# Performance work log

Measured on AMD Instinct MI355X. Metric: run time of the kernel, lower is better.

The kernel has to match this reference:

```python
import jax, jax.numpy as jnp
import numpy as np

N_TREE = 200
DEPTH = 3
N_LEAF = 2 ** (DEPTH + 1) - 1      # 15 internal decision nodes
N_LEAVES = N_LEAF + 1              # 16 leaves
N_NODE = 64
BATCH = 2048
D_FEAT = 512
LR = 0.01


def _leaf_paths(depth):
    """For each of the 2^(depth+1) leaves, the internal-node index and the
    left/right bit at every level (matches the tf.gather index construction:
    bit==0 -> take p, bit==1 -> take 1-p; children of node n are 2n+1, 2n+2)."""
    L = 2 ** (depth + 1)
    nodes = np.zeros((L, depth + 1), np.int32)
    bits = np.zeros((L, depth + 1), np.int32)
    for l in range(L):
        node = 0
        for d in range(depth + 1):
            bit = (l >> (depth - d)) & 1
            nodes[l, d] = node
            bits[l, d] = bit
            node = 2 * node + 1 + bit
    return nodes, bits

_NODES, _BITS = _leaf_paths(DEPTH)


def setup_inputs() -> dict:
    key = jax.random.key(0)
    ks = jax.random.split(key, 9)
    u = lambda k, s: jax.random.uniform(k, s, jnp.float32, -0.05, 0.05)  # keras 'uniform' init
    return {
        "x": jax.random.normal(ks[0], (BATCH, D_FEAT), jnp.float32),
        "y_true": jax.random.normal(ks[1], (BATCH, 1), jnp.float32),
        "w_t": u(ks[2], (N_TREE, D_FEAT, N_NODE)),
        "b_t": u(ks[3], (N_TREE, N_NODE)),
        "w_d": u(ks[4], (N_TREE, N_NODE, N_LEAF)),
        "b_d": u(ks[5], (N_TREE, N_LEAF)),
        "w_l": u(ks[6], (N_TREE, N_LEAVES)),
        "b_l": u(ks[7], (N_TREE,)),
        "f_0": jnp.full((1,), 0.5, jnp.float32),
    }


def reference(x, y_true, w_t, b_t, w_d, b_d, w_l, b_l, f_0):
    B = x.shape[0]
    # Batched per-tree small MLP (the 200-iteration Python loop in the original).
    # Dropout is identity at inference.
    h = jax.nn.relu(jnp.einsum('bd,tdn->tbn', x, w_t) + b_t[:, None, :])        # [T,B,N_NODE]
    p = jax.nn.sigmoid(jnp.einsum('tbn,tnl->tbl', h, w_d) + b_d[:, None, :])    # [T,B,15]
    # Soft binary-tree routing: mu[t,b,leaf] = prod over path of p or (1-p).
    # This reproduces the tiled-index tf.gather construction exactly.
    pn = p[..., _NODES]                                                         # [T,B,16,DEPTH+1]
    q = jnp.where(_BITS == 1, 1.0 - pn, pn)
    mu = jnp.prod(q, axis=-1)                                                   # [T,B,16]
    # Per-tree leaf score with tanh.
    f = jnp.tanh(jnp.einsum('tbl,tl->tb', mu, w_l) + b_l[:, None])              # [T,B]
    # Sequential boosting accumulation: predict_k = f_0 + lr * sum_{i<k} f_i.
    cum = f_0 + LR * jnp.cumsum(f.T, axis=1)                                    # [B,T]
    py_x = jnp.concatenate([jnp.broadcast_to(f_0[None, :], (B, 1)), cum], axis=1)  # [B,T+1]
    return py_x
```

## Files before the change

### kernel.cpp

```cpp
#include <hip/hip_runtime.h>

#define T_TREES 200
#define BATCH   2048
#define D_FEAT  512
#define N_NODE  64
#define LR      0.01f

typedef __attribute__((__ext_vector_type__(8)))  __bf16 bf16x8;
typedef __attribute__((__ext_vector_type__(16))) float  f32x16;

__device__ __forceinline__ unsigned short f32_to_bf16(float f) {
    unsigned u = __float_as_uint(f);
    u += 0x7FFFu + ((u >> 16) & 1u);
    return (unsigned short)(u >> 16);
}

__device__ __forceinline__ void gload_lds16(const void* g, void* l) {
    __builtin_amdgcn_global_load_lds(
        (__attribute__((address_space(1))) void*)(void*)g,
        (__attribute__((address_space(3))) void*)l,
        16, 0, 0);
}

__global__ __launch_bounds__(256) void prep_all(
    const float* __restrict__ x, const float* __restrict__ w_t,
    const float* __restrict__ w_d,
    unsigned short* __restrict__ x_p, unsigned short* __restrict__ w_p,
    unsigned short* __restrict__ w_dt) {
    __shared__ float tile[64 * 65];
    int b = blockIdx.x;
    if (b < 256) {
        int mb = b >> 3, slab = b & 7;
        const float* src = x + (mb * 64) * D_FEAT + slab * 64;
        #pragma unroll
        for (int p = 0; p < 16; ++p) {
            int idx = p * 256 + threadIdx.x;
            int r = idx >> 6, c = idx & 63;
            tile[r * 65 + c] = src[r * D_FEAT + c];
        }
        __syncthreads();
        int mt = mb >> 1, mq = mb & 1;
        unsigned short* dst = x_p + mt * 65536 + slab * 8192 + mq * 512;
        #pragma unroll
        for (int p = 0; p < 2; ++p) {
            int sid = p * 256 + threadIdx.x;
            int kgl = sid >> 6;
            int r   = sid & 63;
            const float* sr = &tile[r * 65 + kgl * 8];
            bf16x8 o;
            #pragma unroll
            for (int j = 0; j < 8; ++j) o[j] = (__bf16)sr[j];
            *(bf16x8*)(dst + kgl * 1024 + r * 8) = o;
        }
    } else if (b < 1856) {
        int bb = b - 256;
        int t = bb >> 3, slab = bb & 7;
        const float* src = w_t + t * (D_FEAT * N_NODE) + slab * 64 * N_NODE;
        #pragma unroll
        for (int p = 0; p < 16; ++p) {
            int idx = p * 256 + threadIdx.x;
            int d = idx >> 6, n = idx & 63;
            tile[d * 65 + n] = src[d * N_NODE + n];
        }
        __syncthreads();
        unsigned short* dst = w_p + (t >> 1) * 65536 + slab * 8192 + (t & 1) * 512;
        #pragma unroll
        for (int p = 0; p < 2; ++p) {
            int sid = p * 256 + threadIdx.x;
            int kgl = sid >> 6;
            int n   = sid & 63;
            bf16x8 o;
            #pragma unroll
            for (int j = 0; j < 8; ++j) o[j] = (__bf16)tile[(kgl * 8 + j) * 65 + n];
            *(bf16x8*)(dst + kgl * 1024 + n * 8) = o;
        }
    } else {
        int i = (b - 1856) * 256 + threadIdx.x;
        int n = i & 63;
        int l = (i >> 6) & 31;
        int t = i >> 11;
        float v = (l < 15) ? w_d[(t * 64 + n) * 15 + l] : 0.f;
        w_dt[i] = f32_to_bf16(v);
    }
}

__global__ __launch_bounds__(256, 4) void gbdt_main(
    const unsigned short* __restrict__ x_p,
    const unsigned short* __restrict__ w_p,
    const unsigned short* __restrict__ w_dt,
    const float* __restrict__ b_t,
    const float* __restrict__ b_d,
    const float* __restrict__ w_l,
    const float* __restrict__ b_l,
    float* __restrict__ f_ws)
{
    __shared__ alignas(16) char smem[34816];
    unsigned short* Hs = (unsigned short*)smem;
    __bf16*         Hb = (__bf16*)smem;
    float*          Pf = (float*)smem;

    const int tid    = threadIdx.x;
    const int lane   = tid & 63;
    const int w      = tid >> 6;
    const int lane31 = lane & 31;
    const int kh     = lane >> 5;
    const int wm     = w >> 1;
    const int wn     = w & 1;

    const int xcd  = blockIdx.x & 7;
    const int slot = blockIdx.x >> 3;
    const int mt   = slot & 15;
    const int pj   = slot >> 4;
    const int pair = xcd * 13 + pj;
    if (pair >= 100) return;
    const int t0 = pair * 2;
    const int m0 = mt * 128;

    const unsigned short* pA = x_p + mt * 65536 + kh * 1024 + (wm * 64 + lane31) * 8;
    const char* gb = (const char*)(w_p + pair * 65536) + tid * 16;

    const int boff = kh * 2048 + (wn * 64 + lane31) * 16;

    f32x16 acc[2][2];
    #pragma unroll
    for (int mb = 0; mb < 2; ++mb)
        #pragma unroll
        for (int nb = 0; nb < 2; ++nb)
            acc[mb][nb] = (f32x16)(0.f);

#define LOAD_A(cn, areg) do {                                      \
        _Pragma("unroll")                                          \
        for (int s2 = 0; s2 < 2; ++s2)                             \
            _Pragma("unroll")                                      \
            for (int mb = 0; mb < 2; ++mb)                         \
                (areg)[s2 * 2 + mb] =                              \
                    *(const bf16x8*)(pA + (cn) * 4096 + s2 * 2048 + mb * 256); \
    } while (0)

#define STAGE_B(cn, base) do {                                            \
        gload_lds16(gb + (cn) * 8192,        (base) + tid * 16);          \
        gload_lds16(gb + (cn) * 8192 + 4096, (base) + tid * 16 + 4096);   \
    } while (0)

    bf16x8 aC[4], aN[4];
    LOAD_A(0, aC);
    STAGE_B(0, smem);
    STAGE_B(1, smem + 8192);

    char* rd  = smem;
    char* rd1 = smem + 8192;
    char* st2 = smem + 16384;

    #pragma unroll
    for (int c = 0; c < 16; ++c) {
        if (c < 15) asm volatile("s_waitcnt vmcnt(2)" ::: "memory");
        else        asm volatile("s_waitcnt vmcnt(0)" ::: "memory");
        __builtin_amdgcn_s_barrier();
        if (c < 15) LOAD_A(c + 1, aN);
        if (c < 14) STAGE_B(c + 2, st2);
        __builtin_amdgcn_s_setprio(1);
        #pragma unroll
        for (int s2 = 0; s2 < 2; ++s2) {
            bf16x8 bv0 = *(const bf16x8*)(rd + boff + s2 * 4096);
            bf16x8 bv1 = *(const bf16x8*)(rd + boff + s2 * 4096 + 512);
            acc[0][0] = __builtin_amdgcn_mfma_f32_32x32x16_bf16(aC[s2 * 2 + 0], bv0, acc[0][0], 0, 0, 0);
            acc[0][1] = __builtin_amdgcn_mfma_f32_32x32x16_bf16(aC[s2 * 2 + 0], bv1, acc[0][1], 0, 0, 0);
            acc[1][0] = __builtin_amdgcn_mfma_f32_32x32x16_bf16(aC[s2 * 2 + 1], bv0, acc[1][0], 0, 0, 0);
            acc[1][1] = __builtin_amdgcn_mfma_f32_32x32x16_bf16(aC[s2 * 2 + 1], bv1, acc[1][1], 0, 0, 0);
        }
        __builtin_amdgcn_s_setprio(0);
        char* t = rd; rd = rd1; rd1 = st2; st2 = t;
        #pragma unroll
        for (int i = 0; i < 4; ++i) aC[i] = aN[i];
    }

    __syncthreads();

    #pragma unroll
    for (int nb = 0; nb < 2; ++nb) {
        float btv = b_t[(t0 + wn) * 64 + nb * 32 + lane31];
        #pragma unroll
        for (int mb = 0; mb < 2; ++mb)
            #pragma unroll
            for (int r = 0; r < 16; ++r) {
                int m = wm * 64 + mb * 32 + (r & 3) + 8 * (r >> 2) + 4 * kh;
                float h = fmaxf(acc[mb][nb][r] + btv, 0.f);
                Hb[wn * 8704 + m * 68 + nb * 32 + lane31] = (__bf16)h;
            }
    }
    __syncthreads();

    f32x16 acc2[2] = { (f32x16)(0.f), (f32x16)(0.f) };
    const unsigned short* pW = w_dt + (t0 + wn) * 2048 + lane31 * 64 + kh * 8;
    __builtin_amdgcn_s_setprio(1);
    #pragma unroll
    for (int s = 0; s < 4; ++s) {
        bf16x8 bv = *(const bf16x8*)(pW + s * 16);
        #pragma unroll
        for (int i = 0; i < 2; ++i) {
            const unsigned short* pH =
                Hs + wn * 8704 + (wm * 64 + i * 32 + lane31) * 68 + s * 16 + kh * 8;
            bf16x8 av = *(const bf16x8*)pH;
            acc2[i] = __builtin_amdgcn_mfma_f32_32x32x16_bf16(av, bv, acc2[i], 0, 0, 0);
        }
    }
    __builtin_amdgcn_s_setprio(0);
    __syncthreads();

    if (lane31 < 15) {
        float bdv = b_d[(t0 + wn) * 15 + lane31];
        #pragma unroll
        for (int i = 0; i < 2; ++i)
            #pragma unroll
            for (int r = 0; r < 16; ++r) {
                int m = wm * 64 + i * 32 + (r & 3) + 8 * (r >> 2) + 4 * kh;
                float lg = acc2[i][r] + bdv;
                Pf[(wn * 128 + m) * 17 + lane31] = 1.f / (1.f + __expf(-lg));
            }
    }
    __syncthreads();

    {
        int m = tid & 127;
        int j = tid >> 7;
        int t = t0 + j;
        float pv[15];
        #pragma unroll
        for (int i = 0; i < 15; ++i) pv[i] = Pf[(j * 128 + m) * 17 + i];
        float facc = 0.f;
        #pragma unroll
        for (int leaf = 0; leaf < 16; ++leaf) {
            float mu = 1.f;
            int node = 0;
            #pragma unroll
            for (int d = 0; d < 4; ++d) {
                int bit = (leaf >> (3 - d)) & 1;
                float p = pv[node];
                mu *= bit ? (1.f - p) : p;
                node = 2 * node + 1 + bit;
            }
            facc += mu * w_l[t * 16 + leaf];
        }
        f_ws[(m0 + m) * T_TREES + t] = tanhf(facc + b_l[t]);
    }
#undef STAGE_B
#undef LOAD_A
}

__global__ __launch_bounds__(256) void scan_k(const float* __restrict__ f_ws,
                                              const float* __restrict__ f0p,
                                              float* __restrict__ out) {
    int lane = threadIdx.x & 63, wid = threadIdx.x >> 6;
    int b = blockIdx.x * 4 + wid;
    float f0 = f0p[0];
    float4 v;
    if (lane < 50) v = *(const float4*)(f_ws + b * T_TREES + lane * 4);
    else           v = make_float4(0.f, 0.f, 0.f, 0.f);
    float p0 = v.x;
    float p1 = p0 + v.y;
    float p2 = p1 + v.z;
    float p3 = p2 + v.w;
    float s = p3;
    #pragma unroll
    for (int off = 1; off < 64; off <<= 1) {
        float y = __shfl_up(s, off, 64);
        if (lane >= off) s += y;
    }
    float excl = s - p3;
    if (lane < 50) {
        float* o = out + b * (T_TREES + 1) + 1 + lane * 4;
        o[0] = f0 + LR * (excl + p0);
        o[1] = f0 + LR * (excl + p1);
        o[2] = f0 + LR * (excl + p2);
        o[3] = f0 + LR * (excl + p3);
    }
    if (lane == 0) out[b * (T_TREES + 1)] = f0;
}

extern "C" void kernel_launch(void* const* d_in, const int* in_sizes, int n_in,
                              void* d_out, int out_size, void* d_ws, size_t ws_size,
                              hipStream_t stream) {
    const float* x   = (const float*)d_in[0];
    const float* w_t = (const float*)d_in[2];
    const float* b_t = (const float*)d_in[3];
    const float* w_d = (const float*)d_in[4];
    const float* b_d = (const float*)d_in[5];
    const float* w_l = (const float*)d_in[6];
    const float* b_l = (const float*)d_in[7];
    const float* f_0 = (const float*)d_in[8];
    float* out = (float*)d_out;

    char* ws = (char*)d_ws;
    unsigned short* x_p  = (unsigned short*)(ws);
    unsigned short* w_p  = (unsigned short*)(ws + 2097152);
    unsigned short* w_dt = (unsigned short*)(ws + 15204352);
    float*          f_ws = (float*)(ws + 16023552);

    prep_all<<<3456, 256, 0, stream>>>(x, w_t, w_d, x_p, w_p, w_dt);
    gbdt_main<<<1664, 256, 0, stream>>>(x_p, w_p, w_dt, b_t, b_d, w_l, b_l, f_ws);
    scan_k<<<512, 256, 0, stream>>>(f_ws, f_0, out);
}
```

Measured before the change: 132.0 us.

## Double the batch rows per block to reuse staged tree weights twice

Each block now covers 256 batch rows instead of 128. Every wave holds four M sub-tiles in registers, so each weight tile staged into LDS feeds twice as many MFMAs, and the grid is halved. The epilogue (bias/relu, second matmul, sigmoid, tree routing, tanh) runs in two halves reusing the same LDS buffers, with output rows remapped to match. Launch bounds drop to two blocks per SM to allow the larger accumulator set, which lowers occupancy and adds register pressure.

```diff
diff --git a/kernel.cpp b/kernel.cpp
--- a/kernel.cpp
+++ b/kernel.cpp
@@ -84,7 +84,7 @@
     }
 }
 
-__global__ __launch_bounds__(256, 4) void gbdt_main(
+__global__ __launch_bounds__(256, 2) void gbdt_main(
     const unsigned short* __restrict__ x_p,
     const unsigned short* __restrict__ w_p,
     const unsigned short* __restrict__ w_dt,
@@ -109,21 +109,21 @@
 
     const int xcd  = blockIdx.x & 7;
     const int slot = blockIdx.x >> 3;
-    const int mt   = slot & 15;
-    const int pj   = slot >> 4;
+    const int mt8  = slot & 7;
+    const int pj   = slot >> 3;
     const int pair = xcd * 13 + pj;
     if (pair >= 100) return;
     const int t0 = pair * 2;
-    const int m0 = mt * 128;
-
-    const unsigned short* pA = x_p + mt * 65536 + kh * 1024 + (wm * 64 + lane31) * 8;
+    const int m0 = mt8 * 256;
+
+    const unsigned short* pA = x_p + (2 * mt8 + wm) * 65536 + kh * 1024 + lane31 * 8;
     const char* gb = (const char*)(w_p + pair * 65536) + tid * 16;
 
     const int boff = kh * 2048 + (wn * 64 + lane31) * 16;
 
-    f32x16 acc[2][2];
-    #pragma unroll
-    for (int mb = 0; mb < 2; ++mb)
+    f32x16 acc[4][2];
+    #pragma unroll
+    for (int mb = 0; mb < 4; ++mb)
         #pragma unroll
         for (int nb = 0; nb < 2; ++nb)
             acc[mb][nb] = (f32x16)(0.f);
@@ -132,8 +132,8 @@
         _Pragma("unroll")                                          \
         for (int s2 = 0; s2 < 2; ++s2)                             \
             _Pragma("unroll")                                      \
-            for (int mb = 0; mb < 2; ++mb)                         \
-                (areg)[s2 * 2 + mb] =                              \
+            for (int mb = 0; mb < 4; ++mb)                         \
+                (areg)[s2 * 4 + mb] =                              \
                     *(const bf16x8*)(pA + (cn) * 4096 + s2 * 2048 + mb * 256); \
     } while (0)
 
@@ -142,7 +142,7 @@
         gload_lds16(gb + (cn) * 8192 + 4096, (base) + tid * 16 + 4096);   \
     } while (0)
 
-    bf16x8 aC[4], aN[4];
+    bf16x8 aC[8], aN[8];
     LOAD_A(0, aC);
     STAGE_B(0, smem);
     STAGE_B(1, smem + 8192);
@@ -163,85 +163,97 @@
         for (int s2 = 0; s2 < 2; ++s2) {
             bf16x8 bv0 = *(const bf16x8*)(rd + boff + s2 * 4096);
             bf16x8 bv1 = *(const bf16x8*)(rd + boff + s2 * 4096 + 512);
-            acc[0][0] = __builtin_amdgcn_mfma_f32_32x32x16_bf16(aC[s2 * 2 + 0], bv0, acc[0][0], 0, 0, 0);
-            acc[0][1] = __builtin_amdgcn_mfma_f32_32x32x16_bf16(aC[s2 * 2 + 0], bv1, acc[0][1], 0, 0, 0);
-            acc[1][0] = __builtin_amdgcn_mfma_f32_32x32x16_bf16(aC[s2 * 2 + 1], bv0, acc[1][0], 0, 0, 0);
-            acc[1][1] = __builtin_amdgcn_mfma_f32_32x32x16_bf16(aC[s2 * 2 + 1], bv1, acc[1][1], 0, 0, 0);
+            #pragma unroll
+            for (int mb = 0; mb < 4; ++mb) {
+                acc[mb][0] = __builtin_amdgcn_mfma_f32_32x32x16_bf16(aC[s2 * 4 + mb], bv0, acc[mb][0], 0, 0, 0);
+                acc[mb][1] = __builtin_amdgcn_mfma_f32_32x32x16_bf16(aC[s2 * 4 + mb], bv1, acc[mb][1], 0, 0, 0);
+            }
         }
         __builtin_amdgcn_s_setprio(0);
         char* t = rd; rd = rd1; rd1 = st2; st2 = t;
         #pragma unroll
-        for (int i = 0; i < 4; ++i) aC[i] = aN[i];
+        for (int i = 0; i < 8; ++i) aC[i] = aN[i];
     }
 
     __syncthreads();
 
-    #pragma unroll
-    for (int nb = 0; nb < 2; ++nb) {
-        float btv = b_t[(t0 + wn) * 64 + nb * 32 + lane31];
-        #pragma unroll
-        for (int mb = 0; mb < 2; ++mb)
-            #pragma unroll
-            for (int r = 0; r < 16; ++r) {
-                int m = wm * 64 + mb * 32 + (r & 3) + 8 * (r >> 2) + 4 * kh;
-                float h = fmaxf(acc[mb][nb][r] + btv, 0.f);
-                Hb[wn * 8704 + m * 68 + nb * 32 + lane31] = (__bf16)h;
+    float btv[2];
+    #pragma unroll
+    for (int nb = 0; nb < 2; ++nb)
+        btv[nb] = b_t[(t0 + wn) * 64 + nb * 32 + lane31];
+
+    #pragma unroll
+    for (int h = 0; h < 2; ++h) {
+        #pragma unroll
+        for (int nb = 0; nb < 2; ++nb) {
+            #pragma unroll
+            for (int q = 0; q < 2; ++q) {
+                int mb = 2 * h + q;
+                #pragma unroll
+                for (int r = 0; r < 16; ++r) {
+                    int m = wm * 64 + q * 32 + (r & 3) + 8 * (r >> 2) + 4 * kh;
+                    float hv = fmaxf(acc[mb][nb][r] + btv[nb], 0.f);
+                    Hb[wn * 8704 + m * 68 + nb * 32 + lane31] = (__bf16)hv;
+                }
             }
-    }
-    __syncthreads();
-
-    f32x16 acc2[2] = { (f32x16)(0.f), (f32x16)(0.f) };
-    const unsigned short* pW = w_dt + (t0 + wn) * 2048 + lane31 * 64 + kh * 8;
-    __builtin_amdgcn_s_setprio(1);
-    #pragma unroll
-    for (int s = 0; s < 4; ++s) {
-        bf16x8 bv = *(const bf16x8*)(pW + s * 16);
-        #pragma unroll
-        for (int i = 0; i < 2; ++i) {
-            const unsigned short* pH =
-                Hs + wn * 8704 + (wm * 64 + i * 32 + lane31) * 68 + s * 16 + kh * 8;
-            bf16x8 av = *(const bf16x8*)pH;
-            acc2[i] = __builtin_amdgcn_mfma_f32_32x32x16_bf16(av, bv, acc2[i], 0, 0, 0);
-        }
-    }
-    __builtin_amdgcn_s_setprio(0);
-    __syncthreads();
-
-    if (lane31 < 15) {
-        float bdv = b_d[(t0 + wn) * 15 + lane31];
-        #pragma unroll
-        for (int i = 0; i < 2; ++i)
-            #pragma unroll
-            for (int r = 0; r < 16; ++r) {
-                int m = wm * 64 + i * 32 + (r & 3) + 8 * (r >> 2) + 4 * kh;
-                float lg = acc2[i][r] + bdv;
-                Pf[(wn * 128 + m) * 17 + lane31] = 1.f / (1.f + __expf(-lg));
+        }
+        __syncthreads();
+
+        f32x16 acc2[2] = { (f32x16)(0.f), (f32x16)(0.f) };
+        const unsigned short* pW = w_dt + (t0 + wn) * 2048 + lane31 * 64 + kh * 8;
+        __builtin_amdgcn_s_setprio(1);
+        #pragma unroll
+        for (int s = 0; s < 4; ++s) {
+            bf16x8 bv = *(const bf16x8*)(pW + s * 16);
+            #pragma unroll
+            for (int i = 0; i < 2; ++i) {
+                const unsigned short* pH =
+                    Hs + wn * 8704 + (wm * 64 + i * 32 + lane31) * 68 + s * 16 + kh * 8;
+                bf16x8 av = *(const bf16x8*)pH;
+                acc2[i] = __builtin_amdgcn_mfma_f32_32x32x16_bf16(av, bv, acc2[i], 0, 0, 0);
             }
-    }
-    __syncthreads();
-
-    {
-        int m = tid & 127;
-        int j = tid >> 7;
-        int t = t0 + j;
-        float pv[15];
-        #pragma unroll
-        for (int i = 0; i < 15; ++i) pv[i] = Pf[(j * 128 + m) * 17 + i];
-        float facc = 0.f;
-        #pragma unroll
-        for (int leaf = 0; leaf < 16; ++leaf) {
-            float mu = 1.f;
-            int node = 0;
-            #pragma unroll
-            for (int d = 0; d < 4; ++d) {
-                int bit = (leaf >> (3 - d)) & 1;
-                float p = pv[node];
-                mu *= bit ? (1.f - p) : p;
-                node = 2 * node + 1 + bit;
+        }
+        __builtin_amdgcn_s_setprio(0);
+        __syncthreads();
+
+        if (lane31 < 15) {
+            float bdv = b_d[(t0 + wn) * 15 + lane31];
+            #pragma unroll
+            for (int i = 0; i < 2; ++i)
+                #pragma unroll
+                for (int r = 0; r < 16; ++r) {
+                    int m = wm * 64 + i * 32 + (r & 3) + 8 * (r >> 2) + 4 * kh;
+                    float lg = acc2[i][r] + bdv;
+                    Pf[(wn * 128 + m) * 17 + lane31] = 1.f / (1.f + __expf(-lg));
+                }
+        }
+        __syncthreads();
+
+        {
+            int m = tid & 127;
+            int j = tid >> 7;
+            int t = t0 + j;
+            float pv[15];
+            #pragma unroll
+            for (int i = 0; i < 15; ++i) pv[i] = Pf[(j * 128 + m) * 17 + i];
+            float facc = 0.f;
+            #pragma unroll
+            for (int leaf = 0; leaf < 16; ++leaf) {
+                float mu = 1.f;
+                int node = 0;
+                #pragma unroll
+                for (int d = 0; d < 4; ++d) {
+                    int bit = (leaf >> (3 - d)) & 1;
+                    float p = pv[node];
+                    mu *= bit ? (1.f - p) : p;
+                    node = 2 * node + 1 + bit;
+                }
+                facc += mu * w_l[t * 16 + leaf];
             }
-            facc += mu * w_l[t * 16 + leaf];
-        }
-        f_ws[(m0 + m) * T_TREES + t] = tanhf(facc + b_l[t]);
+            int g = m0 + (m >> 6) * 128 + h * 64 + (m & 63);
+            f_ws[g * T_TREES + t] = tanhf(facc + b_l[t]);
+        }
+        if (h == 0) __syncthreads();
     }
 #undef STAGE_B
 #undef LOAD_A
@@ -297,6 +309,6 @@
     float*          f_ws = (float*)(ws + 16023552);
 
     prep_all<<<3456, 256, 0, stream>>>(x, w_t, w_d, x_p, w_p, w_dt);
-    gbdt_main<<<1664, 256, 0, stream>>>(x_p, w_p, w_dt, b_t, b_d, w_l, b_l, f_ws);
+    gbdt_main<<<832, 256, 0, stream>>>(x_p, w_p, w_dt, b_t, b_d, w_l, b_l, f_ws);
     scan_k<<<512, 256, 0, stream>>>(f_ws, f_0, out);
 }
```

After: 139.3 us. 1.06x slower.
